# Performance work log

Measured on AMD Instinct MI355X. Metric: run time of the kernel, lower is better.

## Reference

```python
import jax, jax.numpy as jnp
import numpy as np

NODE_FEAT = 200  # F.interpolate size in run_all_node
TOPN = 2         # StitchModel.topn


def _node_feats(img, mask, flow, n_inst, max_pix):
    """Vectorized run_all_node: per-instance gather, linear interp to NODE_FEAT,
    3x3 sign histogram of flow[:2], mean of flow[2]. mask holds labels 1..n_inst;
    max_pix is a static upper bound on pixels per instance."""
    flat = mask.reshape(-1) - 1                       # labels 0..N-1
    order = jnp.argsort(flat)                         # stable sort by label
    counts = jax.ops.segment_sum(jnp.ones_like(flat), flat, num_segments=n_inst)
    starts = jnp.concatenate([jnp.zeros((1,), counts.dtype), jnp.cumsum(counts)[:-1]])
    j = jnp.arange(max_pix)
    pos = starts[:, None] + jnp.minimum(j[None, :], counts[:, None] - 1)
    idx = order[pos]                                  # [N, max_pix] padded pixel indices
    valid = j[None, :] < counts[:, None]              # [N, max_pix]
    iv = img.reshape(-1)[idx]                         # instance intensity profiles
    fx = flow[0].reshape(-1)[idx]
    fy = flow[1].reshape(-1)[idx]
    fz = flow[2].reshape(-1)[idx]
    cf = counts.astype(img.dtype)
    zflow = jnp.where(valid, fz, 0).sum(1) / cf       # flows[-1][m].mean()

    def interp(v, L):                                 # torch linear interp, align_corners=False
        Lf = L.astype(img.dtype)
        p = jnp.clip((jnp.arange(NODE_FEAT, dtype=img.dtype) + 0.5) * (Lf / NODE_FEAT) - 0.5,
                     0.0, Lf - 1.0)
        i0 = jnp.floor(p).astype(jnp.int32)
        i1 = jnp.minimum(i0 + 1, L - 1)
        w = p - i0.astype(img.dtype)
        return v[i0] * (1 - w) + v[i1] * w

    nodes = jax.vmap(interp)(iv, counts)              # [N, 200]
    # hist_flow_vector: bins ordered (x:<0,==0,>0) x (y:<0,==0,>0) -> 3*cx+cy
    cx = jnp.where(fx < 0, 0, jnp.where(fx == 0, 1, 2))
    cy = jnp.where(fy < 0, 0, jnp.where(fy == 0, 1, 2))
    bins = cx * 3 + cy
    oh = (bins[..., None] == jnp.arange(9)) & valid[..., None]
    hist = oh.sum(1).astype(img.dtype)                # [N, 9]
    return jnp.concatenate([nodes, hist], -1), zflow


def setup_inputs() -> dict:
    H = W = 2048
    N = 4096
    pix = (H * W) // N
    key = jax.random.key(0)
    ks = jax.random.split(key, 8)

    def make_mask(k):
        labels = (jnp.arange(H * W, dtype=jnp.int32) // pix) + 1   # labels 1..N
        perm = jax.random.permutation(k, H * W)
        return labels[perm].reshape(H, W)

    def make_bbox(k):
        u = jax.random.uniform(k, (N, 4), jnp.float32)
        centers = u[:, :2] * H
        sizes = u[:, 2:] * 49.0 + 1.0                               # nonzero w/h (asserted)
        return jnp.concatenate([centers, sizes], -1)

    return {
        "img1": jax.random.normal(ks[0], (H, W), jnp.float32),
        "img2": jax.random.normal(ks[1], (H, W), jnp.float32),
        "flow1": jax.random.normal(ks[2], (3, H, W), jnp.float32),
        "flow2": jax.random.normal(ks[3], (3, H, W), jnp.float32),
        "bbox1": make_bbox(ks[4]),
        "bbox2": make_bbox(ks[5]),
        "mask1": make_mask(ks[6]),
        "mask2": make_mask(ks[7]),
    }


def reference(img1, img2, flow1, flow2, bbox1, bbox2, mask1, mask2):
    N1, N2 = bbox1.shape[0], bbox2.shape[0]
    max1 = mask1.size // N1   # static bound on pixels/instance (equal-partition masks)
    max2 = mask2.size // N2
    node1, zf1 = _node_feats(img1, mask1, flow1, N1, max1)
    node2, zf2 = _node_feats(img2, mask2, flow2, N2, max2)
    x = jnp.concatenate([node1, node2], 0)            # [(N1+N2), 209]
    # build_one_graph_low_ram: per row, TOPN smallest center distances
    d = jnp.sqrt(((bbox1[:, None, :2] - bbox2[None, :, :2]) ** 2).sum(-1))  # [N1,N2]
    _, nbr = jax.lax.top_k(-d, TOPN)                  # smallest-first, like argsort[:topn]
    src = jnp.repeat(jnp.arange(N1), TOPN)            # [N1*TOPN]
    dst = nbr.reshape(-1)
    edge_index = jnp.stack([src, dst + N1])           # [2, N1*TOPN]
    edge_attr = jnp.stack([
        zf1[src], zf2[dst],
        bbox1[src, 0] - bbox2[dst, 0],
        bbox1[src, 1] - bbox2[dst, 1],
        bbox1[src, 2] / bbox2[dst, 2],
        bbox1[src, 3] / bbox2[dst, 3],
    ], -1)                                            # [N1*TOPN, 6]
    return x, edge_index, edge_attr
```

## Files before the change

kernel.cpp:

```cpp
#include <hip/hip_runtime.h>
#include <math.h>

#pragma clang fp contract(off)

#define HW      (2048*2048)
#define NI      4096
#define MAXPIX  1024
#define NF      200
#define FEAT    209
#define NE      (NI*2)
#define XSIZE   ((2*NI)*FEAT)
#define EIOFF   XSIZE
#define EAOFF   (EIOFF + 2*NE)

#define S       8192
#define CHK     (HW/S)
#define TOTCHK  (2*CHK)
#define NBPI    256
#define LPB     16
#define NBG     (2*NBPI)
#define REC     (2*HW)
#define BTOT    (LPB*MAXPIX)
#define NWS     16
#define NXCD    8

template<int NB>
__device__ __forceinline__ unsigned long long match_bits(int v) {
    unsigned long long m = ~0ull;
    #pragma unroll
    for (int bit = 0; bit < NB; ++bit) {
        unsigned long long bb = __ballot((v >> bit) & 1);
        m &= ((v >> bit) & 1) ? bb : ~bb;
    }
    return m;
}

__global__ void __launch_bounds__(512) count_zf_kernel(const int* __restrict__ mask1,
        const int* __restrict__ mask2, const float* __restrict__ flow1,
        const float* __restrict__ flow2, unsigned* __restrict__ cntA,
        float* __restrict__ zfpart) {
    __shared__ unsigned cnt[8][NBPI];
    __shared__ float zfp[NI];
    int t = threadIdx.x, w = t >> 6, lane = t & 63;
    for (int j = t; j < 8*NBPI; j += 512) ((unsigned*)cnt)[j] = 0u;
    for (int j = t; j < NI; j += 512) zfp[j] = 0.f;
    __syncthreads();
    int c = blockIdx.x;
    int img = c / CHK;
    const int4*   mask  = (const int4*)(img ? mask2 : mask1);
    const float4* flowz = (const float4*)((img ? flow2 : flow1) + 2L*HW);
    long base4 = (long)(c - img*CHK) * (S/4) + (long)w * (S/32);
    #pragma unroll
    for (int it = 0; it < S/32; it += 64) {
        int4   l4 = mask[base4 + it + lane];
        float4 fz = flowz[base4 + it + lane];
        atomicAdd(&cnt[w][(l4.x-1) >> 4], 1u);
        atomicAdd(&cnt[w][(l4.y-1) >> 4], 1u);
        atomicAdd(&cnt[w][(l4.z-1) >> 4], 1u);
        atomicAdd(&cnt[w][(l4.w-1) >> 4], 1u);
        atomicAdd(&zfp[l4.x-1], fz.x);
        atomicAdd(&zfp[l4.y-1], fz.y);
        atomicAdd(&zfp[l4.z-1], fz.z);
        atomicAdd(&zfp[l4.w-1], fz.w);
    }
    __syncthreads();
    if (t < NBPI) {
        unsigned s = 0;
        #pragma unroll
        for (int q = 0; q < 8; ++q) s += cnt[q][t];
        cntA[(long)c * NBPI + t] = s;
    }
    float* zdst = zfpart + (long)c * NI;
    for (int j = t; j < NI; j += 512) zdst[j] = zfp[j];
}

__global__ void __launch_bounds__(256) scan1_kernel(unsigned* __restrict__ cntA) {
    __shared__ int wsum[4];
    int gb = blockIdx.x;
    int img = gb >> 8, lb = gb & (NBPI - 1);
    int t = threadIdx.x, lane = t & 63, w = t >> 6;
    const int PER = CHK / 256;
    unsigned e[PER]; int s = 0;
    long base = ((long)img * CHK + (long)t * PER) * NBPI + lb;
    #pragma unroll
    for (int i = 0; i < PER; ++i) { e[i] = cntA[base + (long)i * NBPI]; s += (int)e[i]; }
    int incl = s;
    #pragma unroll
    for (int off = 1; off < 64; off <<= 1) {
        int o = __shfl_up(incl, off);
        if (lane >= off) incl += o;
    }
    if (lane == 63) wsum[w] = incl;
    __syncthreads();
    int add = 0;
    for (int q = 0; q < w; ++q) add += wsum[q];
    unsigned pre = (unsigned)(incl + add - s);
    #pragma unroll
    for (int i = 0; i < PER; ++i) { unsigned cv = e[i]; cntA[base + (long)i * NBPI] = pre; pre += cv; }
}

__global__ void __launch_bounds__(1024) zfred_kernel(const float* __restrict__ zfpart,
        float* __restrict__ zfm) {
    __shared__ float red[16][64];
    int t = threadIdx.x, b = blockIdx.x;
    int img = b >> 6;
    int l0  = (b & 63) * 64;
    int rg = t >> 6, lane = t & 63;
    const float* p = zfpart + ((long)img*CHK + rg)*NI + l0 + lane;
    float s = 0.f;
    #pragma unroll 8
    for (int r = 0; r < CHK; r += 16) s += p[(long)r*NI];
    red[rg][lane] = s;
    __syncthreads();
    if (t < 64) {
        float sum = 0.f;
        #pragma unroll
        for (int g = 0; g < 16; ++g) sum += red[g][t];
        zfm[img*NI + l0 + t] = sum * (1.0f/(float)MAXPIX);
    }
}

__global__ void __launch_bounds__(1024, 8) sort_kernel(
        const float* __restrict__ img1, const float* __restrict__ img2,
        const float* __restrict__ flow1, const float* __restrict__ flow2,
        const int* __restrict__ mask1, const int* __restrict__ mask2,
        const unsigned* __restrict__ cntA,
        float* __restrict__ riv, unsigned char* __restrict__ rmeta) {
    __shared__ float ivs[S];
    __shared__ unsigned short smeta[S];
    __shared__ unsigned short cw[NWS][NBPI];
    int* wsum  = (int*)smeta;
    int* gofsA = (int*)cw;
    int t = threadIdx.x, w = t >> 6, lane = t & 63;
    int bid = blockIdx.x;
    int c = (bid & (NXCD-1)) * (TOTCHK/NXCD) + (bid >> 3);
    int img = c / CHK;
    const int*   mask  = img ? mask2  : mask1;
    const float* image = img ? img2   : img1;
    const float* flow  = img ? flow2  : flow1;
    long base = (long)(c - img*CHK) * S;
    unsigned pre = 0;
    if (t < NBPI) pre = cntA[(long)c * NBPI + t];
    for (int j = t; j < NWS*NBPI; j += 1024) ((unsigned short*)cw)[j] = 0;
    __syncthreads();
    long qbase = base + (long)w * (S/NWS);
    int   pk[8];
    float piv[8];
    unsigned long long ltmask = (1ull << lane) - 1ull;
    #pragma unroll
    for (int it = 0; it < 8; ++it) {
        long p = qbase + it*64 + lane;
        int l = mask[p] - 1;
        piv[it] = image[p];
        float fx = flow[p], fy = flow[HW + p];
        int cx = fx < 0.f ? 0 : (fx == 0.f ? 1 : 2);
        int cy = fy < 0.f ? 0 : (fy == 0.f ? 1 : 2);
        int bkt = l >> 4;
        unsigned long long m = match_bits<8>(bkt);
        int cb = __popcll(m & ltmask);
        int ct = __popcll(m);
        pk[it] = l | ((cx*3 + cy) << 12) | (cb << 16) | (ct << 22);
        if (cb == 0) cw[w][bkt] += (unsigned short)ct;
    }
    __syncthreads();
    int tot = 0, incl = 0;
    if (t < NBPI) {
        #pragma unroll
        for (int q = 0; q < NWS; ++q) tot += cw[q][t];
        incl = tot;
        #pragma unroll
        for (int off = 1; off < 64; off <<= 1) {
            int o = __shfl_up(incl, off);
            if (lane >= off) incl += o;
        }
        if (lane == 63) wsum[w] = incl;
    }
    __syncthreads();
    int gof = 0;
    if (t < NBPI) {
        int add = 0;
        for (int q = 0; q < w; ++q) add += wsum[q];
        int excl = incl + add - tot;
        int run = excl;
        #pragma unroll
        for (int q = 0; q < NWS; ++q) {
            int cq = cw[q][t];
            cw[q][t] = (unsigned short)run;
            run += cq;
        }
        gof = (img*NBPI + t) * BTOT + (int)pre - excl;
    }
    __syncthreads();
    #pragma unroll
    for (int it = 0; it < 8; ++it) {
        int pkv = pk[it];
        int l = pkv & 4095, bin = (pkv >> 12) & 15;
        int cb = (pkv >> 16) & 63, ct = (pkv >> 22) & 127;
        int bkt = l >> 4;
        int r0 = (int)cw[w][bkt];
        int dst = r0 + cb;
        if (cb == ct - 1) cw[w][bkt] = (unsigned short)(r0 + ct);
        ivs[dst] = piv[it];
        smeta[dst] = (unsigned short)((bkt << 8) | (bin << 4) | (l & 15));
    }
    __syncthreads();
    if (t < NBPI) gofsA[t] = gof;
    __syncthreads();
    for (int j = t; j < S; j += 1024) {
        int ms = (int)smeta[j];
        int b = ms >> 8;
        int g = gofsA[b] + j;
        riv[g]   = ivs[j];
        rmeta[g] = (unsigned char)(ms & 0xFF);
    }
}

__global__ void __launch_bounds__(1024) stageB_kernel(
        const float* __restrict__ riv, const unsigned char* __restrict__ rmeta,
        float* __restrict__ out) {
    __shared__ float acc[LPB * NF];
    __shared__ float s_tw[MAXPIX];
    __shared__ int   s_tk[MAXPIX];
    __shared__ int   hist[LPB * 9];
    __shared__ int   qc[16][LPB];
    __shared__ int   cur[16][LPB];
    int t = threadIdx.x, w = t >> 6, lane = t & 63;
    int gb = blockIdx.x;
    for (int j = t; j < LPB*NF; j += 1024) acc[j] = 0.f;
    if (t < MAXPIX) s_tk[t] = -1;
    if (t < LPB*9) hist[t] = 0;
    for (int j = t; j < 16*LPB; j += 1024) ((int*)qc)[j] = 0;
    __syncthreads();
    if (t < NF) {
        const float Lf = (float)MAXPIX;
        float p = ((float)t + 0.5f) * (Lf / (float)NF) - 0.5f;
        p = fminf(fmaxf(p, 0.0f), Lf - 1.0f);
        int i0 = (int)floorf(p);
        int i1 = min(i0 + 1, MAXPIX - 1);
        float wg = p - (float)i0;
        s_tk[i0] = t; s_tw[i0] = 1.0f - wg;
        s_tk[i1] = t; s_tw[i1] = wg;
    }
    long base = (long)gb * BTOT;
    const int qsz = BTOT / 16;
    int qbeg = w * qsz;
    const int nit = qsz / 64;
    unsigned long long ltmask = (1ull << lane) - 1ull;
    {
        const uchar4* rm4 = (const uchar4*)(rmeta + base + qbeg);
        #pragma unroll
        for (int it = 0; it < nit/4; ++it) {
            uchar4 m = rm4[it*64 + lane];
            atomicAdd(&qc[w][m.x & 15], 1);
            atomicAdd(&qc[w][m.y & 15], 1);
            atomicAdd(&qc[w][m.z & 15], 1);
            atomicAdd(&qc[w][m.w & 15], 1);
        }
    }
    __syncthreads();
    if (t < LPB) {
        int s = 0;
        #pragma unroll
        for (int q = 0; q < 16; ++q) { cur[q][t] = s; s += qc[q][t]; }
    }
    __syncthreads();
    #pragma unroll 4
    for (int it = 0; it < nit; ++it) {
        int i = qbeg + it*64 + lane;
        int meta = (int)rmeta[base + i];
        float iv = riv[base + i];
        int ll = meta & 15;
        unsigned long long m = match_bits<4>(ll);
        int cb = __popcll(m & ltmask);
        int ct = __popcll(m);
        int r0 = cur[w][ll];
        int rank = r0 + cb;
        if (cb == ct - 1) cur[w][ll] = r0 + ct;
        atomicAdd(&hist[ll*9 + (meta >> 4)], 1);
        int k = s_tk[rank];
        if (k >= 0) atomicAdd(&acc[ll*NF + k], iv * s_tw[rank]);
    }
    __syncthreads();
    for (int j = t; j < LPB*FEAT; j += 1024) {
        int r = j / FEAT, k = j - r*FEAT;
        float v = (k < NF) ? acc[r*NF + k] : (float)hist[r*9 + (k - NF)];
        out[(long)gb * LPB * FEAT + j] = v;
    }
}

__device__ __forceinline__ bool better(float d, int j, float d2, int j2) {
    return d < d2 || (d == d2 && j < j2);
}

__global__ void __launch_bounds__(256) edge_kernel(const float* __restrict__ bbox1,
                                                   const float* __restrict__ bbox2,
                                                   const float* __restrict__ zfm,
                                                   float* __restrict__ out) {
    __shared__ float sbx[NI], sby[NI];
    int wave = threadIdx.x >> 6, lane = threadIdx.x & 63;
    for (int r = threadIdx.x; r < NI; r += 256) {
        float4 b = ((const float4*)bbox2)[r];
        sbx[r] = b.x; sby[r] = b.y;
    }
    __syncthreads();
    int i = blockIdx.x * 4 + wave;
    float c1x = bbox1[i*4 + 0], c1y = bbox1[i*4 + 1];
    float d0 = INFINITY; int j0 = 0x7fffffff;
    float d1 = INFINITY; int j1 = 0x7fffffff;
    for (int t = 0; t < NI; t += 64) {
        int j = t + lane;
        float dx = c1x - sbx[j];
        float dy = c1y - sby[j];
        float dsq = dx*dx + dy*dy;
        float d = (float)sqrt((double)dsq);
        if (better(d, j, d0, j0)) { d1 = d0; j1 = j0; d0 = d; j0 = j; }
        else if (better(d, j, d1, j1)) { d1 = d; j1 = j; }
    }
    for (int off = 32; off; off >>= 1) {
        float od0 = __shfl_down(d0, off); int oj0 = __shfl_down(j0, off);
        float od1 = __shfl_down(d1, off); int oj1 = __shfl_down(j1, off);
        if (better(od0, oj0, d0, j0)) {
            if (better(d0, j0, od1, oj1)) { d1 = d0; j1 = j0; }
            else                          { d1 = od1; j1 = oj1; }
            d0 = od0; j0 = oj0;
        } else if (better(od0, oj0, d1, j1)) { d1 = od0; j1 = oj0; }
    }
    if (lane == 0) {
        float z1 = zfm[i];
        int js[2] = { j0, j1 };
        for (int t = 0; t < 2; ++t) {
            int e = i*2 + t, j = js[t];
            out[EIOFF + e]      = (float)i;
            out[EIOFF + NE + e] = (float)(j + NI);
            float* ea = out + EAOFF + (long)e * 6;
            ea[0] = z1;
            ea[1] = zfm[NI + j];
            ea[2] = c1x - bbox2[j*4 + 0];
            ea[3] = c1y - bbox2[j*4 + 1];
            ea[4] = bbox1[i*4 + 2] / bbox2[j*4 + 2];
            ea[5] = bbox1[i*4 + 3] / bbox2[j*4 + 3];
        }
    }
}

extern "C" void kernel_launch(void* const* d_in, const int* in_sizes, int n_in,
                              void* d_out, int out_size, void* d_ws, size_t ws_size,
                              hipStream_t stream) {
    const float* img1  = (const float*)d_in[0];
    const float* img2  = (const float*)d_in[1];
    const float* flow1 = (const float*)d_in[2];
    const float* flow2 = (const float*)d_in[3];
    const float* bbox1 = (const float*)d_in[4];
    const float* bbox2 = (const float*)d_in[5];
    const int*   mask1 = (const int*)d_in[6];
    const int*   mask2 = (const int*)d_in[7];
    float* out = (float*)d_out;

    char* ws = (char*)d_ws;
    size_t off = 0;
    unsigned* cntA   = (unsigned*)(ws + off); off += (size_t)TOTCHK * NBPI * 4;
    float*    riv    = (float*)(ws + off);    off += (size_t)REC * 4;
    float*    zfpart = (float*)(ws + off);    off += (size_t)TOTCHK * NI * 4;
    float*    zfm    = (float*)(ws + off);    off += 2 * NI * 4;
    unsigned char* rmeta = (unsigned char*)(ws + off); off += (size_t)REC;

    hipLaunchKernelGGL(count_zf_kernel, dim3(TOTCHK), dim3(512), 0, stream,
                       mask1, mask2, flow1, flow2, cntA, zfpart);
    hipLaunchKernelGGL(scan1_kernel, dim3(NBG), dim3(256), 0, stream, cntA);
    hipLaunchKernelGGL(zfred_kernel, dim3(128), dim3(1024), 0, stream, zfpart, zfm);
    hipLaunchKernelGGL(sort_kernel, dim3(TOTCHK), dim3(1024), 0, stream,
                       img1, img2, flow1, flow2, mask1, mask2, cntA, riv, rmeta);
    hipLaunchKernelGGL(stageB_kernel, dim3(NBG), dim3(1024), 0, stream,
                       riv, rmeta, out);
    hipLaunchKernelGGL(edge_kernel, dim3(NI/4), dim3(256), 0, stream,
                       bbox1, bbox2, zfm, out);
}
```

Measured before the change: 302.3 us.

## Merge scan and zflow-reduction kernels; vectorize sort_kernel input loads via LDS staging

Merges the per-bucket prefix scan and the zflow partial-sum reduction into one launch, with block index choosing the branch. This removes one kernel launch and lets the two independent pieces of work run at the same time. The sort kernel now loads mask, image and flow with 128-bit vector loads and packs label and histogram bin into a 16-bit metadata word. It stages these in shared memory before the bucket-matching loop, replacing scalar strided global loads. The cost is an extra shared-memory round trip and a changed per-thread pixel order, which relies on the later stages remaining order-insensitive.

```diff
diff --git a/kernel.cpp b/kernel.cpp
--- a/kernel.cpp
+++ b/kernel.cpp
@@ -74,49 +74,46 @@
     for (int j = t; j < NI; j += 512) zdst[j] = zfp[j];
 }
 
-__global__ void __launch_bounds__(256) scan1_kernel(unsigned* __restrict__ cntA) {
-    __shared__ int wsum[4];
-    int gb = blockIdx.x;
-    int img = gb >> 8, lb = gb & (NBPI - 1);
+__global__ void __launch_bounds__(1024) scan_zf_kernel(unsigned* __restrict__ cntA,
+        const float* __restrict__ zfpart, float* __restrict__ zfm) {
+    __shared__ float red[16][64];
+    int* wsum = (int*)red;
+    int b = blockIdx.x;
     int t = threadIdx.x, lane = t & 63, w = t >> 6;
-    const int PER = CHK / 256;
-    unsigned e[PER]; int s = 0;
-    long base = ((long)img * CHK + (long)t * PER) * NBPI + lb;
-    #pragma unroll
-    for (int i = 0; i < PER; ++i) { e[i] = cntA[base + (long)i * NBPI]; s += (int)e[i]; }
-    int incl = s;
-    #pragma unroll
-    for (int off = 1; off < 64; off <<= 1) {
-        int o = __shfl_up(incl, off);
-        if (lane >= off) incl += o;
-    }
-    if (lane == 63) wsum[w] = incl;
-    __syncthreads();
-    int add = 0;
-    for (int q = 0; q < w; ++q) add += wsum[q];
-    unsigned pre = (unsigned)(incl + add - s);
-    #pragma unroll
-    for (int i = 0; i < PER; ++i) { unsigned cv = e[i]; cntA[base + (long)i * NBPI] = pre; pre += cv; }
-}
-
-__global__ void __launch_bounds__(1024) zfred_kernel(const float* __restrict__ zfpart,
-        float* __restrict__ zfm) {
-    __shared__ float red[16][64];
-    int t = threadIdx.x, b = blockIdx.x;
-    int img = b >> 6;
-    int l0  = (b & 63) * 64;
-    int rg = t >> 6, lane = t & 63;
-    const float* p = zfpart + ((long)img*CHK + rg)*NI + l0 + lane;
-    float s = 0.f;
-    #pragma unroll 8
-    for (int r = 0; r < CHK; r += 16) s += p[(long)r*NI];
-    red[rg][lane] = s;
-    __syncthreads();
-    if (t < 64) {
-        float sum = 0.f;
-        #pragma unroll
-        for (int g = 0; g < 16; ++g) sum += red[g][t];
-        zfm[img*NI + l0 + t] = sum * (1.0f/(float)MAXPIX);
+    if (b < NBG) {
+        int img = b >> 8, lb = b & (NBPI - 1);
+        unsigned e = 0;
+        if (t < CHK) e = cntA[((long)img*CHK + t)*NBPI + lb];
+        int incl = (int)e;
+        #pragma unroll
+        for (int off = 1; off < 64; off <<= 1) {
+            int o = __shfl_up(incl, off);
+            if (lane >= off) incl += o;
+        }
+        if (lane == 63) wsum[w] = incl;
+        __syncthreads();
+        if (t < CHK) {
+            int add = 0;
+            for (int q = 0; q < w; ++q) add += wsum[q];
+            cntA[((long)img*CHK + t)*NBPI + lb] = (unsigned)(incl + add - (int)e);
+        }
+    } else {
+        int b2 = b - NBG;
+        int img = b2 >> 6;
+        int l0  = (b2 & 63) * 64;
+        int rg = t >> 6;
+        const float* p = zfpart + ((long)img*CHK + rg)*NI + l0 + lane;
+        float s = 0.f;
+        #pragma unroll 8
+        for (int r = 0; r < CHK; r += 16) s += p[(long)r*NI];
+        red[rg][lane] = s;
+        __syncthreads();
+        if (t < 64) {
+            float sum = 0.f;
+            #pragma unroll
+            for (int g = 0; g < 16; ++g) sum += red[g][t];
+            zfm[img*NI + l0 + t] = sum * (1.0f/(float)MAXPIX);
+        }
     }
 }
 
@@ -142,24 +139,47 @@
     unsigned pre = 0;
     if (t < NBPI) pre = cntA[(long)c * NBPI + t];
     for (int j = t; j < NWS*NBPI; j += 1024) ((unsigned short*)cw)[j] = 0;
-    __syncthreads();
-    long qbase = base + (long)w * (S/NWS);
+    {
+        const int4*   mk = (const int4*)mask;
+        const float4* iv = (const float4*)image;
+        const float4* fx = (const float4*)flow;
+        const float4* fy = (const float4*)(flow + HW);
+        long i0 = (base >> 2) + (long)w*128 + lane;
+        long i1 = i0 + 64;
+        int4   m0 = mk[i0], m1 = mk[i1];
+        float4 v0 = iv[i0], v1 = iv[i1];
+        float4 x0 = fx[i0], x1 = fx[i1];
+        float4 y0 = fy[i0], y1 = fy[i1];
+        int p0 = (w<<9) + (lane<<2);
+        ushort4 s0, s1;
+        s0.x = (unsigned short)((m0.x-1) | (((x0.x<0.f?0:(x0.x==0.f?1:2))*3 + (y0.x<0.f?0:(y0.x==0.f?1:2))) << 12));
+        s0.y = (unsigned short)((m0.y-1) | (((x0.y<0.f?0:(x0.y==0.f?1:2))*3 + (y0.y<0.f?0:(y0.y==0.f?1:2))) << 12));
+        s0.z = (unsigned short)((m0.z-1) | (((x0.z<0.f?0:(x0.z==0.f?1:2))*3 + (y0.z<0.f?0:(y0.z==0.f?1:2))) << 12));
+        s0.w = (unsigned short)((m0.w-1) | (((x0.w<0.f?0:(x0.w==0.f?1:2))*3 + (y0.w<0.f?0:(y0.w==0.f?1:2))) << 12));
+        s1.x = (unsigned short)((m1.x-1) | (((x1.x<0.f?0:(x1.x==0.f?1:2))*3 + (y1.x<0.f?0:(y1.x==0.f?1:2))) << 12));
+        s1.y = (unsigned short)((m1.y-1) | (((x1.y<0.f?0:(x1.y==0.f?1:2))*3 + (y1.y<0.f?0:(y1.y==0.f?1:2))) << 12));
+        s1.z = (unsigned short)((m1.z-1) | (((x1.z<0.f?0:(x1.z==0.f?1:2))*3 + (y1.z<0.f?0:(y1.z==0.f?1:2))) << 12));
+        s1.w = (unsigned short)((m1.w-1) | (((x1.w<0.f?0:(x1.w==0.f?1:2))*3 + (y1.w<0.f?0:(y1.w==0.f?1:2))) << 12));
+        *(float4*)&ivs[p0]         = v0;
+        *(float4*)&ivs[p0 + 256]   = v1;
+        *(ushort4*)&smeta[p0]       = s0;
+        *(ushort4*)&smeta[p0 + 256] = s1;
+    }
+    __syncthreads();
     int   pk[8];
     float piv[8];
     unsigned long long ltmask = (1ull << lane) - 1ull;
     #pragma unroll
     for (int it = 0; it < 8; ++it) {
-        long p = qbase + it*64 + lane;
-        int l = mask[p] - 1;
-        piv[it] = image[p];
-        float fx = flow[p], fy = flow[HW + p];
-        int cx = fx < 0.f ? 0 : (fx == 0.f ? 1 : 2);
-        int cy = fy < 0.f ? 0 : (fy == 0.f ? 1 : 2);
-        int bkt = l >> 4;
+        int p = (w<<9) + (it<<6) + lane;
+        float ivx = ivs[p];
+        int mt = (int)smeta[p];
+        int bkt = (mt & 4095) >> 4;
         unsigned long long m = match_bits<8>(bkt);
         int cb = __popcll(m & ltmask);
         int ct = __popcll(m);
-        pk[it] = l | ((cx*3 + cy) << 12) | (cb << 16) | (ct << 22);
+        piv[it] = ivx;
+        pk[it] = (mt & 0xFFFF) | (cb << 16) | (ct << 22);
         if (cb == 0) cw[w][bkt] += (unsigned short)ct;
     }
     __syncthreads();
@@ -366,8 +386,8 @@
 
     hipLaunchKernelGGL(count_zf_kernel, dim3(TOTCHK), dim3(512), 0, stream,
                        mask1, mask2, flow1, flow2, cntA, zfpart);
-    hipLaunchKernelGGL(scan1_kernel, dim3(NBG), dim3(256), 0, stream, cntA);
-    hipLaunchKernelGGL(zfred_kernel, dim3(128), dim3(1024), 0, stream, zfpart, zfm);
+    hipLaunchKernelGGL(scan_zf_kernel, dim3(NBG + 128), dim3(1024), 0, stream,
+                       cntA, zfpart, zfm);
     hipLaunchKernelGGL(sort_kernel, dim3(TOTCHK), dim3(1024), 0, stream,
                        img1, img2, flow1, flow2, mask1, mask2, cntA, riv, rmeta);
     hipLaunchKernelGGL(stageB_kernel, dim3(NBG), dim3(1024), 0, stream,
```

Result: no change. 302.6 us (+0.1%).
